# Performance work log

Measured on AMD Instinct MI355X. Metric: run time of the kernel, lower is better.

Reference implementation:

```python
import jax, jax.numpy as jnp
import numpy as np

B, T, I, H, L, C = 256, 512, 128, 256, 2, 1000


def _uniform(key, shape, k):
    return jax.random.uniform(key, shape, jnp.float32, -k, k)


def setup_inputs() -> dict:
    key = jax.random.key(0)
    ks = jax.random.split(key, 12)
    k = 1.0 / np.sqrt(H)
    return {
        "x": jax.random.normal(ks[0], (B, T, I), jnp.float32),
        # layer 0 (PyTorch LSTM param layout: W_ih [4H, in], W_hh [4H, H], biases [4H])
        "Wih0": _uniform(ks[1], (4 * H, I), k),
        "Whh0": _uniform(ks[2], (4 * H, H), k),
        "bih0": _uniform(ks[3], (4 * H,), k),
        "bhh0": _uniform(ks[4], (4 * H,), k),
        # layer 1
        "Wih1": _uniform(ks[5], (4 * H, H), k),
        "Whh1": _uniform(ks[6], (4 * H, H), k),
        "bih1": _uniform(ks[7], (4 * H,), k),
        "bhh1": _uniform(ks[8], (4 * H,), k),
        # final classifier
        "fcW": _uniform(ks[9], (C, H), k),
        "fcb": _uniform(ks[10], (C,), k),
    }


def _lstm_layer(seq, Wih, Whh, bias):
    # seq: [B, T, in]; returns hidden sequence [B, T, H]
    b, t = seq.shape[0], seq.shape[1]
    h_dim = Whh.shape[1]
    # Precompute input projection for all timesteps (one big GEMM).
    x_proj = jnp.einsum('bti,gi->btg', seq, Wih) + bias  # [B, T, 4H]

    def step(carry, xp):
        h, c = carry
        gates = xp + h @ Whh.T                     # [B, 4H]
        i, f, g, o = jnp.split(gates, 4, axis=-1)  # PyTorch gate order i,f,g,o
        i = jax.nn.sigmoid(i)
        f = jax.nn.sigmoid(f)
        g = jnp.tanh(g)
        o = jax.nn.sigmoid(o)
        c = f * c + i * g
        h = o * jnp.tanh(c)
        return (h, c), h

    h0 = jnp.zeros((b, h_dim), seq.dtype)
    c0 = jnp.zeros((b, h_dim), seq.dtype)
    _, hs = jax.lax.scan(step, (h0, c0), jnp.swapaxes(x_proj, 0, 1))  # [T, B, H]
    return jnp.swapaxes(hs, 0, 1)


def reference(x, Wih0, Whh0, bih0, bhh0, Wih1, Whh1, bih1, bhh1, fcW, fcb):
    out = _lstm_layer(x, Wih0, Whh0, bih0 + bhh0)
    out = _lstm_layer(out, Wih1, Whh1, bih1 + bhh1)
    # classifier on last timestep
    return out[:, -1, :] @ fcW.T + fcb  # [B, C]
```

## Files before the change

### kernel.cpp

```cpp
#include <hip/hip_runtime.h>

#define B_ 256
#define T_ 512
#define I_ 128
#define H_ 256
#define C_ 1000

__device__ __forceinline__ float fsig(float x) { return 1.0f / (1.0f + __expf(-x)); }
__device__ __forceinline__ float ftanh(float x) { return 2.0f / (1.0f + __expf(-2.0f * x)) - 1.0f; }

__global__ __launch_bounds__(256) void lstm_step(
    const float* __restrict__ x,
    const float* __restrict__ Wih0, const float* __restrict__ Whh0,
    const float* __restrict__ bih0, const float* __restrict__ bhh0,
    const float* __restrict__ Wih1, const float* __restrict__ Whh1,
    const float* __restrict__ bih1, const float* __restrict__ bhh1,
    float* __restrict__ ws, int s)
{
    __shared__ float As[128 * 36];
    __shared__ float Wsh[128 * 36];

    float* h0buf = ws;
    float* h1buf = ws + 2 * B_ * H_;
    float* c0 = ws + 4 * B_ * H_;
    float* c1 = ws + 5 * B_ * H_;

    const int w = blockIdx.x;
    const int layer = w >> 8;
    const int r = w & 255;
    const int bb = r >> 5;
    const int hb = r & 31;

    if (layer == 0 && s >= T_) return;
    if (layer == 1 && s < 1) return;
    const int t = (layer == 0) ? s : (s - 1);

    const float* hprev; const float* h0cur = nullptr;
    float* hout; float* cbuf;
    const float* Wih; const float* Whh; const float* bi; const float* bh;
    int nchunks;
    if (layer == 0) {
        hprev = h0buf + ((t - 1) & 1) * B_ * H_;
        hout  = h0buf + (t & 1) * B_ * H_;
        cbuf = c0; Wih = Wih0; Whh = Whh0; bi = bih0; bh = bhh0;
        nchunks = 3;
    } else {
        h0cur = h0buf + (t & 1) * B_ * H_;
        hprev = h1buf + ((t - 1) & 1) * B_ * H_;
        hout  = h1buf + (t & 1) * B_ * H_;
        cbuf = c1; Wih = Wih1; Whh = Whh1; bi = bih1; bh = bhh1;
        nchunks = 4;
    }

    const int tid = threadIdx.x;
    const int srow = tid >> 3;
    const int kv = tid & 7;
    const int wave = tid >> 6;
    const int lane = tid & 63;
    const int br = lane >> 3;
    const int gc8 = lane & 7;
    const int grow = (srow >> 3) * H_ + hb * 8 + (srow & 7);

    float acc[4][4];
#pragma unroll
    for (int a = 0; a < 4; ++a)
#pragma unroll
        for (int b = 0; b < 4; ++b) acc[a][b] = 0.0f;

    for (int cc = 0; cc < nchunks; ++cc) {
        const float* ap;
        const float* wp;
        if (layer == 0) {
            if (cc == 0) { ap = x + ((size_t)(bb * 32 + srow) * T_ + t) * I_; wp = Wih + grow * I_; }
            else         { ap = hprev + (bb * 32 + srow) * H_ + (cc - 1) * 128; wp = Whh + grow * H_ + (cc - 1) * 128; }
        } else {
            if (cc < 2)  { ap = h0cur + (bb * 32 + srow) * H_ + cc * 128;       wp = Wih + grow * H_ + cc * 128; }
            else         { ap = hprev + (bb * 32 + srow) * H_ + (cc - 2) * 128; wp = Whh + grow * H_ + (cc - 2) * 128; }
        }
#pragma unroll
        for (int i = 0; i < 4; ++i) {
            const int k4 = (kv + 8 * i) * 4;
            float4 va = *(const float4*)(ap + k4);
            As[(k4 + 0) * 36 + srow] = va.x;
            As[(k4 + 1) * 36 + srow] = va.y;
            As[(k4 + 2) * 36 + srow] = va.z;
            As[(k4 + 3) * 36 + srow] = va.w;
            float4 vw = *(const float4*)(wp + k4);
            Wsh[(k4 + 0) * 36 + srow] = vw.x;
            Wsh[(k4 + 1) * 36 + srow] = vw.y;
            Wsh[(k4 + 2) * 36 + srow] = vw.z;
            Wsh[(k4 + 3) * 36 + srow] = vw.w;
        }
        __syncthreads();
        const float* Ap = &As[(wave * 32) * 36 + br * 4];
        const float* Wp = &Wsh[(wave * 32) * 36 + gc8 * 4];
#pragma unroll
        for (int kk = 0; kk < 32; ++kk) {
            float4 a = *(const float4*)(Ap + kk * 36);
            float4 wv = *(const float4*)(Wp + kk * 36);
            acc[0][0] += a.x * wv.x; acc[0][1] += a.x * wv.y; acc[0][2] += a.x * wv.z; acc[0][3] += a.x * wv.w;
            acc[1][0] += a.y * wv.x; acc[1][1] += a.y * wv.y; acc[1][2] += a.y * wv.z; acc[1][3] += a.y * wv.w;
            acc[2][0] += a.z * wv.x; acc[2][1] += a.z * wv.y; acc[2][2] += a.z * wv.z; acc[2][3] += a.z * wv.w;
            acc[3][0] += a.w * wv.x; acc[3][1] += a.w * wv.y; acc[3][2] += a.w * wv.z; acc[3][3] += a.w * wv.w;
        }
        __syncthreads();
    }

    float* red = As;
    {
        const int base = tid * 16;
#pragma unroll
        for (int a = 0; a < 4; ++a)
#pragma unroll
            for (int b = 0; b < 4; ++b)
                red[base + a * 4 + b] = acc[a][b];
    }
    __syncthreads();
    {
        const int bl = tid >> 3;
        const int j = tid & 7;
        float g4[4];
#pragma unroll
        for (int g = 0; g < 4; ++g) {
            const int gc = g * 8 + j;
            const int br2 = bl >> 2, bi2 = bl & 3, gq = gc >> 2, gj = gc & 3;
            float v = 0.0f;
#pragma unroll
            for (int wv = 0; wv < 4; ++wv)
                v += red[(wv * 64 + br2 * 8 + gq) * 16 + bi2 * 4 + gj];
            const int growg = g * H_ + hb * 8 + j;
            v += bi[growg] + bh[growg];
            g4[g] = v;
        }
        const float ig = fsig(g4[0]);
        const float fg = fsig(g4[1]);
        const float gg = ftanh(g4[2]);
        const float og = fsig(g4[3]);
        const int b = bb * 32 + bl;
        const int hidx = hb * 8 + j;
        const int ci = b * H_ + hidx;
        const float cn = fg * cbuf[ci] + ig * gg;
        cbuf[ci] = cn;
        hout[ci] = og * ftanh(cn);
    }
}

__global__ __launch_bounds__(256) void fc_kernel(
    const float* __restrict__ ws, const float* __restrict__ fcW,
    const float* __restrict__ fcb, float* __restrict__ out)
{
    __shared__ float As[128 * 36];
    __shared__ float Wsh[128 * 36];

    const float* h1 = ws + 3 * B_ * H_;
    const int bb = blockIdx.x >> 5;
    const int cb = blockIdx.x & 31;
    const int tid = threadIdx.x;
    const int srow = tid >> 3;
    const int kv = tid & 7;
    const int wave = tid >> 6;
    const int lane = tid & 63;
    const int br = lane >> 3;
    const int gc8 = lane & 7;
    const int crow = cb * 32 + srow;

    float acc[4][4];
#pragma unroll
    for (int a = 0; a < 4; ++a)
#pragma unroll
        for (int b = 0; b < 4; ++b) acc[a][b] = 0.0f;

    for (int cc = 0; cc < 2; ++cc) {
        const float* ap = h1 + (bb * 32 + srow) * H_ + cc * 128;
#pragma unroll
        for (int i = 0; i < 4; ++i) {
            const int k4 = (kv + 8 * i) * 4;
            float4 va = *(const float4*)(ap + k4);
            As[(k4 + 0) * 36 + srow] = va.x;
            As[(k4 + 1) * 36 + srow] = va.y;
            As[(k4 + 2) * 36 + srow] = va.z;
            As[(k4 + 3) * 36 + srow] = va.w;
            float4 vw = make_float4(0.f, 0.f, 0.f, 0.f);
            if (crow < C_) vw = *(const float4*)(fcW + crow * H_ + cc * 128 + k4);
            Wsh[(k4 + 0) * 36 + srow] = vw.x;
            Wsh[(k4 + 1) * 36 + srow] = vw.y;
            Wsh[(k4 + 2) * 36 + srow] = vw.z;
            Wsh[(k4 + 3) * 36 + srow] = vw.w;
        }
        __syncthreads();
        const float* Ap = &As[(wave * 32) * 36 + br * 4];
        const float* Wp = &Wsh[(wave * 32) * 36 + gc8 * 4];
#pragma unroll
        for (int kk = 0; kk < 32; ++kk) {
            float4 a = *(const float4*)(Ap + kk * 36);
            float4 wv = *(const float4*)(Wp + kk * 36);
            acc[0][0] += a.x * wv.x; acc[0][1] += a.x * wv.y; acc[0][2] += a.x * wv.z; acc[0][3] += a.x * wv.w;
            acc[1][0] += a.y * wv.x; acc[1][1] += a.y * wv.y; acc[1][2] += a.y * wv.z; acc[1][3] += a.y * wv.w;
            acc[2][0] += a.z * wv.x; acc[2][1] += a.z * wv.y; acc[2][2] += a.z * wv.z; acc[2][3] += a.z * wv.w;
            acc[3][0] += a.w * wv.x; acc[3][1] += a.w * wv.y; acc[3][2] += a.w * wv.z; acc[3][3] += a.w * wv.w;
        }
        __syncthreads();
    }

    float* red = As;
    {
        const int base = tid * 16;
#pragma unroll
        for (int a = 0; a < 4; ++a)
#pragma unroll
            for (int b = 0; b < 4; ++b)
                red[base + a * 4 + b] = acc[a][b];
    }
    __syncthreads();
    {
        const int bl = tid >> 3;
        const int j = tid & 7;
#pragma unroll
        for (int g = 0; g < 4; ++g) {
            const int gc = g * 8 + j;
            const int br2 = bl >> 2, bi2 = bl & 3, gq = gc >> 2, gj = gc & 3;
            float v = 0.0f;
#pragma unroll
            for (int wv = 0; wv < 4; ++wv)
                v += red[(wv * 64 + br2 * 8 + gq) * 16 + bi2 * 4 + gj];
            const int cglob = cb * 32 + gc;
            if (cglob < C_) {
                v += fcb[cglob];
                out[(size_t)(bb * 32 + bl) * C_ + cglob] = v;
            }
        }
    }
}

extern "C" void kernel_launch(void* const* d_in, const int* in_sizes, int n_in,
                              void* d_out, int out_size, void* d_ws, size_t ws_size,
                              hipStream_t stream)
{
    const float* x    = (const float*)d_in[0];
    const float* Wih0 = (const float*)d_in[1];
    const float* Whh0 = (const float*)d_in[2];
    const float* bih0 = (const float*)d_in[3];
    const float* bhh0 = (const float*)d_in[4];
    const float* Wih1 = (const float*)d_in[5];
    const float* Whh1 = (const float*)d_in[6];
    const float* bih1 = (const float*)d_in[7];
    const float* bhh1 = (const float*)d_in[8];
    const float* fcW  = (const float*)d_in[9];
    const float* fcb  = (const float*)d_in[10];
    float* ws  = (float*)d_ws;
    float* out = (float*)d_out;

    hipMemsetAsync(d_ws, 0, (size_t)6 * B_ * H_ * sizeof(float), stream);

    for (int s = 0; s <= T_; ++s) {
        lstm_step<<<512, 256, 0, stream>>>(x, Wih0, Whh0, bih0, bhh0,
                                           Wih1, Whh1, bih1, bhh1, ws, s);
    }
    fc_kernel<<<256, 256, 0, stream>>>(ws, fcW, fcb, out);
}
```

Baseline: 7.506 ms.

## Double-buffer LDS chunks with register prefetch and row-major k-split tiles

Replaces the transposed scalar LDS stores with row-major float4 stores into a double-buffered LDS area, and prefetches the next K-chunk into registers while the current chunk is computed. This cuts one barrier per chunk. The four waves now split along K within each chunk rather than along the previous mapping, and the reduction is rewritten to use float4 reads with a padded stride and gate-interleaved accumulators. The goal is fewer LDS bank conflicts and better overlap of global loads with FMA work, at the cost of more registers and a larger LDS footprint.

Result: slower. 14.51 ms (+93.3%).

```diff
diff --git a/kernel.cpp b/kernel.cpp
--- a/kernel.cpp
+++ b/kernel.cpp
@@ -5,6 +5,9 @@
 #define I_ 128
 #define H_ 256
 #define C_ 1000
+
+#define LDSTR 132
+#define RSTR  20
 
 __device__ __forceinline__ float fsig(float x) { return 1.0f / (1.0f + __expf(-x)); }
 __device__ __forceinline__ float ftanh(float x) { return 2.0f / (1.0f + __expf(-2.0f * x)) - 1.0f; }
@@ -17,8 +20,7 @@
     const float* __restrict__ bih1, const float* __restrict__ bhh1,
     float* __restrict__ ws, int s)
 {
-    __shared__ float As[128 * 36];
-    __shared__ float Wsh[128 * 36];
+    __shared__ float lds[4 * 32 * LDSTR];
 
     float* h0buf = ws;
     float* h1buf = ws + 2 * B_ * H_;
@@ -61,85 +63,123 @@
     const int gc8 = lane & 7;
     const int grow = (srow >> 3) * H_ + hb * 8 + (srow & 7);
 
+    auto a_src = [&](int cc) -> const float* {
+        if (layer == 0) {
+            if (cc == 0) return x + ((size_t)(bb * 32 + srow) * T_ + t) * I_;
+            return hprev + (bb * 32 + srow) * H_ + (cc - 1) * 128;
+        }
+        if (cc < 2) return h0cur + (bb * 32 + srow) * H_ + cc * 128;
+        return hprev + (bb * 32 + srow) * H_ + (cc - 2) * 128;
+    };
+    auto w_src = [&](int cc) -> const float* {
+        if (layer == 0) {
+            if (cc == 0) return Wih + grow * I_;
+            return Whh + grow * H_ + (cc - 1) * 128;
+        }
+        if (cc < 2) return Wih + grow * H_ + cc * 128;
+        return Whh + grow * H_ + (cc - 2) * 128;
+    };
+
     float acc[4][4];
 #pragma unroll
     for (int a = 0; a < 4; ++a)
 #pragma unroll
         for (int b = 0; b < 4; ++b) acc[a][b] = 0.0f;
 
+    float4 ra[4], rw[4];
+
+    {
+        const float* ap = a_src(0);
+        const float* wp = w_src(0);
+#pragma unroll
+        for (int m = 0; m < 4; ++m) {
+            ra[m] = *(const float4*)(ap + (kv + 8 * m) * 4);
+            rw[m] = *(const float4*)(wp + (kv + 8 * m) * 4);
+        }
+        float* ad = lds + srow * LDSTR;
+        float* wd = lds + 32 * LDSTR + srow * LDSTR;
+#pragma unroll
+        for (int m = 0; m < 4; ++m) {
+            *(float4*)(ad + (kv + 8 * m) * 4) = ra[m];
+            *(float4*)(wd + (kv + 8 * m) * 4) = rw[m];
+        }
+    }
+    __syncthreads();
+
     for (int cc = 0; cc < nchunks; ++cc) {
-        const float* ap;
-        const float* wp;
-        if (layer == 0) {
-            if (cc == 0) { ap = x + ((size_t)(bb * 32 + srow) * T_ + t) * I_; wp = Wih + grow * I_; }
-            else         { ap = hprev + (bb * 32 + srow) * H_ + (cc - 1) * 128; wp = Whh + grow * H_ + (cc - 1) * 128; }
-        } else {
-            if (cc < 2)  { ap = h0cur + (bb * 32 + srow) * H_ + cc * 128;       wp = Wih + grow * H_ + cc * 128; }
-            else         { ap = hprev + (bb * 32 + srow) * H_ + (cc - 2) * 128; wp = Whh + grow * H_ + (cc - 2) * 128; }
-        }
-#pragma unroll
-        for (int i = 0; i < 4; ++i) {
-            const int k4 = (kv + 8 * i) * 4;
-            float4 va = *(const float4*)(ap + k4);
-            As[(k4 + 0) * 36 + srow] = va.x;
-            As[(k4 + 1) * 36 + srow] = va.y;
-            As[(k4 + 2) * 36 + srow] = va.z;
-            As[(k4 + 3) * 36 + srow] = va.w;
-            float4 vw = *(const float4*)(wp + k4);
-            Wsh[(k4 + 0) * 36 + srow] = vw.x;
-            Wsh[(k4 + 1) * 36 + srow] = vw.y;
-            Wsh[(k4 + 2) * 36 + srow] = vw.z;
-            Wsh[(k4 + 3) * 36 + srow] = vw.w;
+        const int d = cc & 1;
+        const bool pf = (cc + 1 < nchunks);
+        if (pf) {
+            const float* ap = a_src(cc + 1);
+            const float* wp = w_src(cc + 1);
+#pragma unroll
+            for (int m = 0; m < 4; ++m) {
+                ra[m] = *(const float4*)(ap + (kv + 8 * m) * 4);
+                rw[m] = *(const float4*)(wp + (kv + 8 * m) * 4);
+            }
+        }
+        const float* Ab = lds + (d * 2) * 32 * LDSTR;
+        const float* Wb = lds + (d * 2 + 1) * 32 * LDSTR;
+#pragma unroll
+        for (int kk = 0; kk < 8; ++kk) {
+            const int co = (wave * 8 + kk) * 4;
+            float4 a0 = *(const float4*)(Ab + (br +  0) * LDSTR + co);
+            float4 a1 = *(const float4*)(Ab + (br +  8) * LDSTR + co);
+            float4 a2 = *(const float4*)(Ab + (br + 16) * LDSTR + co);
+            float4 a3 = *(const float4*)(Ab + (br + 24) * LDSTR + co);
+            float4 w0 = *(const float4*)(Wb + (gc8 +  0) * LDSTR + co);
+            float4 w1 = *(const float4*)(Wb + (gc8 +  8) * LDSTR + co);
+            float4 w2 = *(const float4*)(Wb + (gc8 + 16) * LDSTR + co);
+            float4 w3 = *(const float4*)(Wb + (gc8 + 24) * LDSTR + co);
+#define DOT4(ACC, A, W) ACC += A.x * W.x; ACC += A.y * W.y; ACC += A.z * W.z; ACC += A.w * W.w;
+            DOT4(acc[0][0], a0, w0) DOT4(acc[0][1], a0, w1) DOT4(acc[0][2], a0, w2) DOT4(acc[0][3], a0, w3)
+            DOT4(acc[1][0], a1, w0) DOT4(acc[1][1], a1, w1) DOT4(acc[1][2], a1, w2) DOT4(acc[1][3], a1, w3)
+            DOT4(acc[2][0], a2, w0) DOT4(acc[2][1], a2, w1) DOT4(acc[2][2], a2, w2) DOT4(acc[2][3], a2, w3)
+            DOT4(acc[3][0], a3, w0) DOT4(acc[3][1], a3, w1) DOT4(acc[3][2], a3, w2) DOT4(acc[3][3], a3, w3)
+#undef DOT4
+        }
+        if (pf) {
+            float* ad = lds + ((d ^ 1) * 2) * 32 * LDSTR + srow * LDSTR;
+            float* wd = lds + ((d ^ 1) * 2 + 1) * 32 * LDSTR + srow * LDSTR;
+#pragma unroll
+            for (int m = 0; m < 4; ++m) {
+                *(float4*)(ad + (kv + 8 * m) * 4) = ra[m];
+                *(float4*)(wd + (kv + 8 * m) * 4) = rw[m];
+            }
         }
         __syncthreads();
-        const float* Ap = &As[(wave * 32) * 36 + br * 4];
-        const float* Wp = &Wsh[(wave * 32) * 36 + gc8 * 4];
-#pragma unroll
-        for (int kk = 0; kk < 32; ++kk) {
-            float4 a = *(const float4*)(Ap + kk * 36);
-            float4 wv = *(const float4*)(Wp + kk * 36);
-            acc[0][0] += a.x * wv.x; acc[0][1] += a.x * wv.y; acc[0][2] += a.x * wv.z; acc[0][3] += a.x * wv.w;
-            acc[1][0] += a.y * wv.x; acc[1][1] += a.y * wv.y; acc[1][2] += a.y * wv.z; acc[1][3] += a.y * wv.w;
-            acc[2][0] += a.z * wv.x; acc[2][1] += a.z * wv.y; acc[2][2] += a.z * wv.z; acc[2][3] += a.z * wv.w;
-            acc[3][0] += a.w * wv.x; acc[3][1] += a.w * wv.y; acc[3][2] += a.w * wv.z; acc[3][3] += a.w * wv.w;
-        }
-        __syncthreads();
-    }
-
-    float* red = As;
-    {
-        const int base = tid * 16;
-#pragma unroll
-        for (int a = 0; a < 4; ++a)
-#pragma unroll
-            for (int b = 0; b < 4; ++b)
-                red[base + a * 4 + b] = acc[a][b];
+    }
+
+    float* red = lds;
+    {
+        const int base = (wave * 64 + lane) * RSTR;
+#pragma unroll
+        for (int i = 0; i < 4; ++i)
+            *(float4*)(red + base + i * 4) =
+                make_float4(acc[i][0], acc[i][1], acc[i][2], acc[i][3]);
     }
     __syncthreads();
     {
-        const int bl = tid >> 3;
-        const int j = tid & 7;
-        float g4[4];
-#pragma unroll
-        for (int g = 0; g < 4; ++g) {
-            const int gc = g * 8 + j;
-            const int br2 = bl >> 2, bi2 = bl & 3, gq = gc >> 2, gj = gc & 3;
-            float v = 0.0f;
-#pragma unroll
-            for (int wv = 0; wv < 4; ++wv)
-                v += red[(wv * 64 + br2 * 8 + gq) * 16 + bi2 * 4 + gj];
-            const int growg = g * H_ + hb * 8 + j;
-            v += bi[growg] + bh[growg];
-            g4[g] = v;
-        }
-        const float ig = fsig(g4[0]);
-        const float fg = fsig(g4[1]);
-        const float gg = ftanh(g4[2]);
-        const float og = fsig(g4[3]);
-        const int b = bb * 32 + bl;
-        const int hidx = hb * 8 + j;
+        const int lp = tid & 63;
+        const int iw = tid >> 6;
+        float4 v = *(const float4*)(red + lp * RSTR + iw * 4);
+#pragma unroll
+        for (int wv = 1; wv < 4; ++wv) {
+            float4 u = *(const float4*)(red + (wv * 64 + lp) * RSTR + iw * 4);
+            v.x += u.x; v.y += u.y; v.z += u.z; v.w += u.w;
+        }
+        const int hidx = hb * 8 + (lp & 7);
+        const float gi = v.x + (bi[hidx] + bh[hidx]);
+        const float gf = v.y + (bi[H_ + hidx] + bh[H_ + hidx]);
+        const float gg = v.z + (bi[2 * H_ + hidx] + bh[2 * H_ + hidx]);
+        const float go = v.w + (bi[3 * H_ + hidx] + bh[3 * H_ + hidx]);
+        const float ig = fsig(gi);
+        const float fg = fsig(gf);
+        const float gn = ftanh(gg);
+        const float og = fsig(go);
+        const int b = bb * 32 + iw * 8 + (lp >> 3);
         const int ci = b * H_ + hidx;
-        const float cn = fg * cbuf[ci] + ig * gg;
+        const float cn = fg * cbuf[ci] + ig * gn;
         cbuf[ci] = cn;
         hout[ci] = og * ftanh(cn);
     }
```
